# Kernel optimization log

Measured on AMD Instinct MI355X. Metric: run time of the kernel, lower is better.

Reference implementation:

```python
import jax, jax.numpy as jnp
import numpy as np

H = 2048          # hidden size
N_HEADS = 16
HEAD_DIM = H // N_HEADS   # 128
ATTN_SCALE = 8.0          # attention_scale > 1.0 -> custom max-subtract path
B, S = 2, 2048


def setup_inputs() -> dict:
    key = jax.random.key(0)
    k1, k2, k3, k4, k5 = jax.random.split(key, 5)
    hidden_states = jax.random.normal(k1, (B, S, H), dtype=jnp.float32)
    # causal left-to-right multiplicative mask, broadcast over batch and heads
    ltor_mask = jnp.tril(jnp.ones((S, S), dtype=jnp.float32))[None, None]
    std = 0.02
    W_qkv = jax.random.normal(k2, (H, 3 * H), dtype=jnp.float32) * std
    b_qkv = jnp.zeros((3 * H,), dtype=jnp.float32)
    W_out = jax.random.normal(k3, (H, H), dtype=jnp.float32) * std
    b_out = jnp.zeros((H,), dtype=jnp.float32)
    return {"hidden_states": hidden_states, "ltor_mask": ltor_mask,
            "W_qkv": W_qkv, "b_qkv": b_qkv, "W_out": W_out, "b_out": b_out}


def reference(hidden_states, ltor_mask, W_qkv, b_qkv, W_out, b_out):
    b, s, h = hidden_states.shape
    # fused QKV projection: [b, s, 3h]
    qkv = jnp.einsum('bsh,hk->bsk', hidden_states, W_qkv) + b_qkv
    q, k, v = jnp.split(qkv, 3, axis=-1)
    # [b, s, h] -> [b, n, s, hn]
    def to_heads(t):
        return t.reshape(b, s, N_HEADS, HEAD_DIM).transpose(0, 2, 1, 3)
    q, k, v = to_heads(q), to_heads(k), to_heads(v)
    # custom scale: q / sqrt(scale), k / sqrt(hn * scale)
    inv = 1.0 / (ATTN_SCALE * np.sqrt(np.float32(HEAD_DIM)))
    scores = jnp.einsum('bnqd,bnkd->bnqk', q, k) * jnp.float32(inv)
    # multiplicative mask BEFORE max-subtract (zeroes masked positions)
    scores = scores * ltor_mask
    # attention_scale > 1.0 path: subtract row max, re-multiply by scale
    scores = (scores - jnp.max(scores, axis=-1, keepdims=True)) * jnp.float32(ATTN_SCALE)
    # additive large-negative fill on masked entries
    scores = scores + jnp.float32(-65504.0) * (1.0 - ltor_mask)
    probs = jax.nn.softmax(scores, axis=-1)
    ctx = jnp.einsum('bnqk,bnkd->bnqd', probs, v)
    ctx = ctx.transpose(0, 2, 1, 3).reshape(b, s, h)
    out = jnp.einsum('bsh,hk->bsk', ctx, W_out) + b_out
    return out
```

## Files before the change

kernel.cpp:

```cpp
#include <hip/hip_runtime.h>

#define S_LEN 2048
#define HDIM  2048
#define NHEADS 16
#define DHEAD 128
#define BATCH 2
#define MROWS (BATCH * S_LEN)
#define QKVN  (3 * HDIM)

typedef _Float16 f16;
typedef _Float16 f16x8 __attribute__((ext_vector_type(8)));
typedef _Float16 f16x4 __attribute__((ext_vector_type(4)));
typedef float    f32x4 __attribute__((ext_vector_type(4)));
typedef float    f32x16 __attribute__((ext_vector_type(16)));

typedef const __attribute__((address_space(1))) void* gas_ptr;
typedef __attribute__((address_space(3))) void*       las_ptr;

#define MFMA16(a, b, c)  __builtin_amdgcn_mfma_f32_16x16x32_f16(a, b, c, 0, 0, 0)
#define MFMA32(a, b, c)  __builtin_amdgcn_mfma_f32_32x32x16_f16(a, b, c, 0, 0, 0)

__device__ __forceinline__ void gl_lds16(const f16* g, f16* lds_wave_base) {
#if defined(__has_builtin) && __has_builtin(__builtin_amdgcn_global_load_lds)
  __builtin_amdgcn_global_load_lds((gas_ptr)g, (las_ptr)lds_wave_base, 16, 0, 0);
#else
  int lane = threadIdx.x & 63;
  ((f16x8*)lds_wave_base)[lane] = *(const f16x8*)g;
#endif
}


__device__ __forceinline__ void transpose_tile(const float* __restrict__ W,
                                               f16* __restrict__ Wb,
                                               int K, int N, int k0, int n0,
                                               float* tile ) {
  int tr = threadIdx.x >> 4;
  int tc = (threadIdx.x & 15) * 4;
  int KT = K >> 5;
#pragma unroll
  for (int rr = 0; rr < 4; ++rr) {
    int r = rr * 16 + tr;
    float4 v = *(const float4*)(W + (size_t)(k0 + r) * N + n0 + tc);
    tile[r * 65 + tc + 0] = v.x; tile[r * 65 + tc + 1] = v.y;
    tile[r * 65 + tc + 2] = v.z; tile[r * 65 + tc + 3] = v.w;
  }
  __syncthreads();
#pragma unroll
  for (int rr = 0; rr < 4; ++rr) {
    int r = rr * 16 + tr;
    int n = n0 + r;
    int kBase = k0 + tc;
    f16x4 o;
#pragma unroll
    for (int c = 0; c < 4; ++c) o[c] = (f16)tile[(tc + c) * 65 + r];
    int nt = n >> 7, nn = n & 127;
    int kt = kBase >> 5, kc = (kBase >> 3) & 3, j = kBase & 7;
    *(f16x4*)(Wb + ((size_t)nt * KT + kt) * 4096 + (kc * 128 + nn) * 8 + j) = o;
  }
}

__global__ __launch_bounds__(256) void prep_kernel(const float* __restrict__ X,
                                                   f16* __restrict__ Xb,
                                                   const float* __restrict__ Wqkv,
                                                   f16* __restrict__ Wqkvb,
                                                   const float* __restrict__ Wout,
                                                   f16* __restrict__ Woutb) {
  __shared__ float tile[64 * 65];
  int bz = blockIdx.x;
  if (bz < 2048) {
    int kt = bz & 63, rt = bz >> 6;
    int t = threadIdx.x;
    int m = t >> 1, half = t & 1;
    const float* src = X + (size_t)(rt * 128 + m) * HDIM + kt * 32 + half * 16;
    float4 v0 = ((const float4*)src)[0];
    float4 v1 = ((const float4*)src)[1];
    float4 v2 = ((const float4*)src)[2];
    float4 v3 = ((const float4*)src)[3];
    f16x8 a = {(f16)v0.x, (f16)v0.y, (f16)v0.z, (f16)v0.w,
               (f16)v1.x, (f16)v1.y, (f16)v1.z, (f16)v1.w};
    f16x8 b = {(f16)v2.x, (f16)v2.y, (f16)v2.z, (f16)v2.w,
               (f16)v3.x, (f16)v3.y, (f16)v3.z, (f16)v3.w};
    f16* dst = Xb + ((size_t)rt * 64 + kt) * 4096 + ((half * 2) * 128 + m) * 8;
    *(f16x8*)dst = a;
    *(f16x8*)(dst + 1024) = b;
  } else if (bz < 5120) {
    int u = bz - 2048;
    int nx = u % 96, ky = u / 96;
    transpose_tile(Wqkv, Wqkvb, HDIM, QKVN, ky * 64, nx * 64, tile);
  } else {
    int u = bz - 5120;
    int nx = u & 31, ky = u >> 5;
    transpose_tile(Wout, Woutb, HDIM, HDIM, ky * 64, nx * 64, tile);
  }
}

template <int MODE>
__global__ __launch_bounds__(256) void gemm_kernel(const f16* __restrict__ Ablk,
                                                   const f16* __restrict__ Bblk,
                                                   const float* __restrict__ bias,
                                                   f16* __restrict__ Cpart,
                                                   f16* __restrict__ Qr,
                                                   f16* __restrict__ KB,
                                                   f16* __restrict__ VB,
                                                   int moff, int M, int N, int K) {
  __shared__ f16 As[4 * 128 * 8];
  __shared__ f16 Bs[4 * 128 * 8];
  int tid = threadIdx.x;
  int lane = tid & 63, w = tid >> 6;
  int lhi = lane >> 4, llo = lane & 15;
  int by = moff + blockIdx.y;
  int m0 = by * 128, n0 = blockIdx.x * 128;
  int wm = (w & 1) * 64, wn = (w >> 1) * 64;
  int KT = K >> 5;
  const f16* Ab = Ablk + (size_t)by * KT * 4096;
  const f16* Bb = Bblk + (size_t)blockIdx.x * KT * 4096;

  int ktBeg = 0, ktEnd = KT;
  if (MODE == 2) { int half = KT >> 1; ktBeg = blockIdx.z * half; ktEnd = ktBeg + half; }

  f32x4 acc[4][4];
#pragma unroll
  for (int i = 0; i < 4; ++i)
#pragma unroll
    for (int j = 0; j < 4; ++j) acc[i][j] = (f32x4){0.f, 0.f, 0.f, 0.f};

  for (int kt = ktBeg; kt < ktEnd; ++kt) {
    __syncthreads();
#pragma unroll
    for (int i2 = 0; i2 < 2; ++i2) {
      int Lw = i2 * 256 + w * 64;
      gl_lds16(Ab + (size_t)kt * 4096 + Lw * 8 + (lane * 8), As + Lw * 8);
      gl_lds16(Bb + (size_t)kt * 4096 + Lw * 8 + (lane * 8), Bs + Lw * 8);
    }
    __syncthreads();

    f16x8 af[4], bf[4];
#pragma unroll
    for (int i = 0; i < 4; ++i)
      af[i] = *(const f16x8*)(As + (lhi * 128 + wm + i * 16 + llo) * 8);
#pragma unroll
    for (int j = 0; j < 4; ++j)
      bf[j] = *(const f16x8*)(Bs + (lhi * 128 + wn + j * 16 + llo) * 8);
#pragma unroll
    for (int i = 0; i < 4; ++i)
#pragma unroll
      for (int j = 0; j < 4; ++j) acc[i][j] = MFMA16(af[i], bf[j], acc[i][j]);
  }

#pragma unroll
  for (int j = 0; j < 4; ++j) {
    int col = n0 + wn + j * 16 + llo;
    float bv = (MODE == 1) ? bias[col] : 0.f;
#pragma unroll
    for (int i = 0; i < 4; ++i) {
      int rowb = m0 + wm + i * 16 + lhi * 4;
      if (MODE == 2) {
        size_t zoff = (size_t)blockIdx.z * M * N;
#pragma unroll
        for (int r = 0; r < 4; ++r)
          Cpart[zoff + (size_t)(rowb + r) * N + col] = (f16)acc[i][j][r];
      } else {
        int region = n0 >> 11;
        if (region == 0) {
#pragma unroll
          for (int r = 0; r < 4; ++r)
            Qr[(size_t)(rowb + r) * HDIM + col] = (f16)(acc[i][j][r] + bv);
        } else if (region == 1) {
          int cK = col - HDIM;
          int hd = cK >> 7, d = cK & 127, g = d >> 3, dj = d & 7;
#pragma unroll
          for (int r = 0; r < 4; ++r) {
            int row = rowb + r;
            int b = row >> 11, s = row & 2047;
            int kt2 = s >> 6, key = s & 63;
            size_t addr = ((((size_t)(b * 16 + hd) * 32 + kt2) * 16 + g) * 64 + key) * 8 + dj;
            KB[addr] = (f16)(acc[i][j][r] + bv);
          }
        } else {
          int cV = col - 2 * HDIM;
          int hd = cV >> 7, d = cV & 127;
          int row = rowb;
          int b = row >> 11, s = row & 2047;
          int kt2 = s >> 6, key = s & 63;
          int kg = key >> 3, kj = key & 7;
          f16x4 pv = {(f16)(acc[i][j][0] + bv), (f16)(acc[i][j][1] + bv),
                      (f16)(acc[i][j][2] + bv), (f16)(acc[i][j][3] + bv)};
          size_t addr = ((((size_t)(b * 16 + hd) * 32 + kt2) * 8 + kg) * 128 + d) * 8 + kj;
          *(f16x4*)(VB + addr) = pv;
        }
      }
    }
  }
}

__global__ __launch_bounds__(256) void merge_out_kernel(const f16* __restrict__ Cpart,
                                                        const float* __restrict__ bias,
                                                        float* __restrict__ out) {
  int t = blockIdx.x * 256 + threadIdx.x;
  int col8 = (t & 255) * 8;
  int row = t >> 8;
  size_t base = (size_t)row * HDIM + col8;
  const size_t MN = (size_t)MROWS * HDIM;
  f16x8 a = *(const f16x8*)(Cpart + base);
  f16x8 b = *(const f16x8*)(Cpart + MN + base);
  float4 b0 = *(const float4*)(bias + col8);
  float4 b1 = *(const float4*)(bias + col8 + 4);
  float4 o0 = {(float)a[0] + (float)b[0] + b0.x, (float)a[1] + (float)b[1] + b0.y,
               (float)a[2] + (float)b[2] + b0.z, (float)a[3] + (float)b[3] + b0.w};
  float4 o1 = {(float)a[4] + (float)b[4] + b1.x, (float)a[5] + (float)b[5] + b1.y,
               (float)a[6] + (float)b[6] + b1.z, (float)a[7] + (float)b[7] + b1.w};
  *(float4*)(out + base) = o0;
  *(float4*)(out + base + 4) = o1;
}

__global__ __launch_bounds__(256, 3) void attn_kernel(const f16* __restrict__ Qr,
                                                      const f16* __restrict__ KB,
                                                      const f16* __restrict__ VB,
                                                      f16* __restrict__ Opart,
                                                      float* __restrict__ Lpart) {
  __shared__ f16 Ks[1024 * 8];
  __shared__ f16 Vs[1024 * 8];
  __shared__ f16 Ps[4][32 * 72];

  int tid = threadIdx.x, lane = tid & 63, w = tid >> 6;
  int l5 = lane & 31, hl = lane >> 5;
  int bh = blockIdx.y, b = bh >> 4, hd = bh & 15;
  int gx = blockIdx.x;
  int qt, kt0, kt1, slot;
  if (gx < 8) { qt = gx; slot = 0; kt0 = 0; kt1 = 2 * qt + 2; }
  else {
    qt = 8 + ((gx - 8) >> 1); slot = (gx - 8) & 1;
    kt0 = slot ? (qt + 1) : 0;
    kt1 = slot ? (2 * qt + 2) : (qt + 1);
  }

  int qbase = qt * 128 + w * 32;
  int qrow = qbase + l5;

  const f16* qp = Qr + (size_t)(b * S_LEN + qrow) * HDIM + hd * DHEAD + hl * 8;
  f16x8 qf[8];
#pragma unroll
  for (int s8 = 0; s8 < 8; ++s8) qf[s8] = *(const f16x8*)(qp + s8 * 16);

  f32x16 oac[4];
#pragma unroll
  for (int mt = 0; mt < 4; ++mt)
#pragma unroll
    for (int r = 0; r < 16; ++r) oac[mt][r] = 0.f;
  float rs = 0.f;

  const float C1 = 0.12752747419986393f;
  const float C2 = 11.541560327111708f;

  const f16* KBb = KB + (size_t)bh * 32 * 8192;
  const f16* VBb = VB + (size_t)bh * 32 * 8192;

  for (int kt = kt0; kt < kt1; ++kt) {
    __syncthreads();
    {
      const f16* Kt = KBb + (size_t)kt * 8192;
      const f16* Vt = VBb + (size_t)kt * 8192;
#pragma unroll
      for (int c = 0; c < 4; ++c) {
        int u0 = w * 256 + c * 64;
        gl_lds16(Kt + (size_t)(u0 + lane) * 8, Ks + u0 * 8);
        gl_lds16(Vt + (size_t)(u0 + lane) * 8, Vs + u0 * 8);
      }
    }
    __syncthreads();

    if (kt * 64 <= qbase + 31) {
      f32x16 sac[2];
#pragma unroll
      for (int mt = 0; mt < 2; ++mt)
#pragma unroll
        for (int r = 0; r < 16; ++r) sac[mt][r] = 0.f;
#pragma unroll
      for (int s8 = 0; s8 < 8; ++s8) {
#pragma unroll
        for (int mt = 0; mt < 2; ++mt) {
          f16x8 kf = *(const f16x8*)(Ks + ((s8 * 2 + hl) * 64 + mt * 32 + l5) * 8);
          sac[mt] = MFMA32(kf, qf[s8], sac[mt]);
        }
      }

      bool diag = (kt * 64 + 63 > qbase);
#pragma unroll
      for (int mt = 0; mt < 2; ++mt) {
#pragma unroll
        for (int g4 = 0; g4 < 4; ++g4) {
          f16x4 pk;
#pragma unroll
          for (int r = 0; r < 4; ++r) {
            int keyl = mt * 32 + g4 * 8 + hl * 4 + r;
            float p = __builtin_amdgcn_exp2f(fmaf(sac[mt][g4 * 4 + r], C1, -C2));
            if (diag && (kt * 64 + keyl > qrow)) p = 0.f;
            rs += p;
            pk[r] = (f16)p;
          }
          *(f16x4*)(&Ps[w][l5 * 72 + mt * 32 + g4 * 8 + hl * 4]) = pk;
        }
      }
      asm volatile("s_waitcnt lgkmcnt(0)" ::: "memory");

#pragma unroll
      for (int ks = 0; ks < 4; ++ks) {
        f16x8 pf = *(const f16x8*)(&Ps[w][l5 * 72 + ks * 16 + hl * 8]);
#pragma unroll
        for (int mt = 0; mt < 4; ++mt) {
          f16x8 vf = *(const f16x8*)(Vs + ((ks * 2 + hl) * 128 + mt * 32 + l5) * 8);
          oac[mt] = MFMA32(vf, pf, oac[mt]);
        }
      }
    }
  }

  float lsum = rs + __shfl_xor(rs, 32, 64);
  size_t ob = ((size_t)slot * 32 + bh) * S_LEN * DHEAD + (size_t)qrow * DHEAD;
#pragma unroll
  for (int mt = 0; mt < 4; ++mt) {
#pragma unroll
    for (int g4 = 0; g4 < 4; ++g4) {
      int d = mt * 32 + g4 * 8 + hl * 4;
      f16x4 ov = {(f16)oac[mt][g4 * 4 + 0], (f16)oac[mt][g4 * 4 + 1],
                  (f16)oac[mt][g4 * 4 + 2], (f16)oac[mt][g4 * 4 + 3]};
      *(f16x4*)(Opart + ob + d) = ov;
    }
  }
  if (hl == 0) Lpart[((size_t)slot * 32 + bh) * S_LEN + qrow] = lsum;
}

__global__ __launch_bounds__(256) void merge_kernel(const f16* __restrict__ Opart,
                                                    const float* __restrict__ Lpart,
                                                    f16* __restrict__ CTXb) {
  int t = blockIdx.x * 256 + threadIdx.x;
  int d8 = (t & 15) * 8;
  int q = (t >> 4) & 2047;
  int bh = t >> 15;
  int b = bh >> 4, hd = bh & 15;
  int ns = ((q >> 7) >= 8) ? 2 : 1;
  size_t o0 = ((size_t)bh * S_LEN + q) * DHEAD + d8;
  const size_t OSLOT = (size_t)32 * S_LEN * DHEAD;
  float l = Lpart[(size_t)bh * S_LEN + q];
  f16x8 a = *(const f16x8*)(Opart + o0);
  float acc[8];
#pragma unroll
  for (int j = 0; j < 8; ++j) acc[j] = (float)a[j];
  if (ns == 2) {
    l += Lpart[OSLOT / DHEAD + (size_t)bh * S_LEN + q];
    f16x8 a2 = *(const f16x8*)(Opart + OSLOT + o0);
#pragma unroll
    for (int j = 0; j < 8; ++j) acc[j] += (float)a2[j];
  }
  float inv = 1.0f / l;
  f16x8 o;
#pragma unroll
  for (int j = 0; j < 8; ++j) o[j] = (f16)(acc[j] * inv);
  int row = b * S_LEN + q;
  int col = hd * DHEAD + d8;
  int rt = row >> 7, rr = row & 127;
  int kt = col >> 5, kc = (col >> 3) & 3;
  *(f16x8*)(CTXb + ((size_t)rt * 64 + kt) * 4096 + (kc * 128 + rr) * 8) = o;
}

extern "C" void kernel_launch(void* const* d_in, const int* in_sizes, int n_in,
                              void* d_out, int out_size, void* d_ws, size_t ws_size,
                              hipStream_t stream) {
  const float* X    = (const float*)d_in[0];
  const float* Wqkv = (const float*)d_in[2];
  const float* bqkv = (const float*)d_in[3];
  const float* Wout = (const float*)d_in[4];
  const float* bout = (const float*)d_in[5];
  float* out = (float*)d_out;

  char* ws = (char*)d_ws;
  f16* Xb    = (f16*)ws;  ws += (size_t)MROWS * HDIM * sizeof(f16);
  f16* Wqkvb = (f16*)ws;  ws += (size_t)QKVN * HDIM * sizeof(f16);
  f16* Woutb = (f16*)ws;  ws += (size_t)HDIM * HDIM * sizeof(f16);
  f16* Qr    = (f16*)ws;  ws += (size_t)MROWS * HDIM * sizeof(f16);
  f16* KB    = (f16*)ws;  ws += (size_t)32 * 32 * 8192 * sizeof(f16);
  f16* VB    = (f16*)ws;  ws += (size_t)32 * 32 * 8192 * sizeof(f16);
  f16* Opart = (f16*)ws;  ws += (size_t)2 * 32 * S_LEN * DHEAD * sizeof(f16);
  float* Lpart = (float*)ws;  ws += (size_t)2 * 32 * S_LEN * sizeof(float);
  f16* CTXb  = Xb;
  f16* Cpart = Opart;

  prep_kernel<<<6144, 256, 0, stream>>>(X, Xb, Wqkv, Wqkvb, Wout, Woutb);

  gemm_kernel<1><<<dim3(QKVN / 128, 16), 256, 0, stream>>>(
      Xb, Wqkvb, bqkv, nullptr, Qr, KB, VB, 0, MROWS, QKVN, HDIM);
  gemm_kernel<1><<<dim3(QKVN / 128, 16), 256, 0, stream>>>(
      Xb, Wqkvb, bqkv, nullptr, Qr, KB, VB, 16, MROWS, QKVN, HDIM);

  attn_kernel<<<dim3(24, 32), 256, 0, stream>>>(Qr, KB, VB, Opart, Lpart);

  merge_kernel<<<(32 * S_LEN * 16) / 256, 256, 0, stream>>>(Opart, Lpart, CTXb);

  gemm_kernel<2><<<dim3(HDIM / 128, 32, 2), 256, 0, stream>>>(
      CTXb, Woutb, nullptr, Cpart, nullptr, nullptr, nullptr, 0, MROWS, HDIM, HDIM);

  merge_out_kernel<<<(MROWS * HDIM / 8) / 256, 256, 0, stream>>>(Cpart, bout, out);
}
```

Baseline: 425.4 us.

## Replace 128x128 GEMM with 256x256 tile, 4-stage async LDS pipeline

Swaps the GEMM kernel for a 512-thread, 256x256 output tile version. Global-to-LDS loads go through a 4-deep ring buffer with explicit vmcnt waits, interleaved barriers and raised wave priority around the MFMA sections. The QKV projection becomes a single launch instead of two half launches. This aims to cut global traffic per FLOP and hide load latency behind MFMA. The cost is much more LDS and more registers per block, which lowers occupancy, and fewer blocks for the output GEMM (256 blocks).

```diff
diff --git a/kernel.cpp b/kernel.cpp
--- a/kernel.cpp
+++ b/kernel.cpp
@@ -21,12 +21,7 @@
 #define MFMA32(a, b, c)  __builtin_amdgcn_mfma_f32_32x32x16_f16(a, b, c, 0, 0, 0)
 
 __device__ __forceinline__ void gl_lds16(const f16* g, f16* lds_wave_base) {
-#if defined(__has_builtin) && __has_builtin(__builtin_amdgcn_global_load_lds)
   __builtin_amdgcn_global_load_lds((gas_ptr)g, (las_ptr)lds_wave_base, 16, 0, 0);
-#else
-  int lane = threadIdx.x & 63;
-  ((f16x8*)lds_wave_base)[lane] = *(const f16x8*)g;
-#endif
 }
 
 
@@ -95,72 +90,107 @@
 }
 
 template <int MODE>
-__global__ __launch_bounds__(256) void gemm_kernel(const f16* __restrict__ Ablk,
-                                                   const f16* __restrict__ Bblk,
-                                                   const float* __restrict__ bias,
-                                                   f16* __restrict__ Cpart,
-                                                   f16* __restrict__ Qr,
-                                                   f16* __restrict__ KB,
-                                                   f16* __restrict__ VB,
-                                                   int moff, int M, int N, int K) {
-  __shared__ f16 As[4 * 128 * 8];
-  __shared__ f16 Bs[4 * 128 * 8];
-  int tid = threadIdx.x;
-  int lane = tid & 63, w = tid >> 6;
-  int lhi = lane >> 4, llo = lane & 15;
-  int by = moff + blockIdx.y;
-  int m0 = by * 128, n0 = blockIdx.x * 128;
-  int wm = (w & 1) * 64, wn = (w >> 1) * 64;
-  int KT = K >> 5;
-  const f16* Ab = Ablk + (size_t)by * KT * 4096;
-  const f16* Bb = Bblk + (size_t)blockIdx.x * KT * 4096;
-
-  int ktBeg = 0, ktEnd = KT;
-  if (MODE == 2) { int half = KT >> 1; ktBeg = blockIdx.z * half; ktEnd = ktBeg + half; }
-
-  f32x4 acc[4][4];
-#pragma unroll
-  for (int i = 0; i < 4; ++i)
+__global__ __launch_bounds__(512, 2) void gemm256_kernel(const f16* __restrict__ Ablk,
+                                                         const f16* __restrict__ Bblk,
+                                                         const float* __restrict__ bias,
+                                                         f16* __restrict__ Cpart,
+                                                         f16* __restrict__ Qr,
+                                                         f16* __restrict__ KB,
+                                                         f16* __restrict__ VB,
+                                                         int M, int N, int K) {
+  __shared__ f16 As[4][2][4096];
+  __shared__ f16 Bs[4][2][4096];
+  const int tid = threadIdx.x;
+  const int lane = tid & 63, wv = tid >> 6;
+  const int lhi = lane >> 4, llo = lane & 15;
+  const int wr = wv >> 2, wc = wv & 3;
+  const int bx = blockIdx.x, by = blockIdx.y;
+  const int KT = K >> 5;
+  int t0 = 0, ntiles = KT;
+  if (MODE == 2) { ntiles = KT >> 1; t0 = blockIdx.z * ntiles; }
+
+  const f16* Ab0 = Ablk + ((size_t)(2 * by)     * KT + t0) * 4096;
+  const f16* Ab1 = Ablk + ((size_t)(2 * by + 1) * KT + t0) * 4096;
+  const f16* Bb0 = Bblk + ((size_t)(2 * bx)     * KT + t0) * 4096;
+  const f16* Bb1 = Bblk + ((size_t)(2 * bx + 1) * KT + t0) * 4096;
+
+  f32x4 acc[8][4];
+#pragma unroll
+  for (int i = 0; i < 8; ++i)
 #pragma unroll
     for (int j = 0; j < 4; ++j) acc[i][j] = (f32x4){0.f, 0.f, 0.f, 0.f};
 
-  for (int kt = ktBeg; kt < ktEnd; ++kt) {
-    __syncthreads();
-#pragma unroll
-    for (int i2 = 0; i2 < 2; ++i2) {
-      int Lw = i2 * 256 + w * 64;
-      gl_lds16(Ab + (size_t)kt * 4096 + Lw * 8 + (lane * 8), As + Lw * 8);
-      gl_lds16(Bb + (size_t)kt * 4096 + Lw * 8 + (lane * 8), Bs + Lw * 8);
-    }
-    __syncthreads();
-
-    f16x8 af[4], bf[4];
+  auto stA = [&](int bufi, int kt) {
+    gl_lds16(Ab0 + (size_t)kt * 4096 + tid * 8, &As[bufi][0][0] + wv * 512);
+    gl_lds16(Ab1 + (size_t)kt * 4096 + tid * 8, &As[bufi][1][0] + wv * 512);
+  };
+  auto stB = [&](int bufi, int kt) {
+    gl_lds16(Bb0 + (size_t)kt * 4096 + tid * 8, &Bs[bufi][0][0] + wv * 512);
+    gl_lds16(Bb1 + (size_t)kt * 4096 + tid * 8, &Bs[bufi][1][0] + wv * 512);
+  };
+
+#pragma unroll
+  for (int u = 0; u < 3; ++u) { stA(u, u); stB(u, u); }
+
+  for (int t = 0; t < ntiles; ++t) {
+    const int buf = t & 3;
+    const bool st = (t + 3 < ntiles);
+    const int nb = (t + 3) & 3, ntile = t + 3;
+
+    if (t + 2 < ntiles)      asm volatile("s_waitcnt vmcnt(8)" ::: "memory");
+    else if (t + 1 < ntiles) asm volatile("s_waitcnt vmcnt(4)" ::: "memory");
+    else                     asm volatile("s_waitcnt vmcnt(0)" ::: "memory");
+    __builtin_amdgcn_s_barrier();
+
+    const f16* Ah = &As[buf][wr][0];
+    const f16* Bh = &Bs[buf][wc >> 1][0];
+    f16x8 bfr[4], afr[4];
+
+#pragma unroll
+    for (int j = 0; j < 4; ++j)
+      bfr[j] = *(const f16x8*)(Bh + (lhi * 128 + (wc & 1) * 64 + j * 16 + llo) * 8);
 #pragma unroll
     for (int i = 0; i < 4; ++i)
-      af[i] = *(const f16x8*)(As + (lhi * 128 + wm + i * 16 + llo) * 8);
-#pragma unroll
-    for (int j = 0; j < 4; ++j)
-      bf[j] = *(const f16x8*)(Bs + (lhi * 128 + wn + j * 16 + llo) * 8);
+      afr[i] = *(const f16x8*)(Ah + (lhi * 128 + i * 16 + llo) * 8);
+    if (st) stA(nb, ntile);
+    __builtin_amdgcn_s_barrier();
+    asm volatile("s_waitcnt lgkmcnt(0)" ::: "memory");
+    __builtin_amdgcn_s_setprio(1);
 #pragma unroll
     for (int i = 0; i < 4; ++i)
 #pragma unroll
-      for (int j = 0; j < 4; ++j) acc[i][j] = MFMA16(af[i], bf[j], acc[i][j]);
+      for (int j = 0; j < 4; ++j) acc[i][j] = MFMA16(afr[i], bfr[j], acc[i][j]);
+    __builtin_amdgcn_s_setprio(0);
+    __builtin_amdgcn_s_barrier();
+
+#pragma unroll
+    for (int i = 0; i < 4; ++i)
+      afr[i] = *(const f16x8*)(Ah + (lhi * 128 + (i + 4) * 16 + llo) * 8);
+    if (st) stB(nb, ntile);
+    __builtin_amdgcn_s_barrier();
+    asm volatile("s_waitcnt lgkmcnt(0)" ::: "memory");
+    __builtin_amdgcn_s_setprio(1);
+#pragma unroll
+    for (int i = 0; i < 4; ++i)
+#pragma unroll
+      for (int j = 0; j < 4; ++j) acc[i + 4][j] = MFMA16(afr[i], bfr[j], acc[i + 4][j]);
+    __builtin_amdgcn_s_setprio(0);
   }
 
 #pragma unroll
   for (int j = 0; j < 4; ++j) {
-    int col = n0 + wn + j * 16 + llo;
+    int col = bx * 256 + wc * 64 + j * 16 + llo;
     float bv = (MODE == 1) ? bias[col] : 0.f;
 #pragma unroll
-    for (int i = 0; i < 4; ++i) {
-      int rowb = m0 + wm + i * 16 + lhi * 4;
+    for (int i = 0; i < 8; ++i) {
+      int rowb = by * 256 + wr * 128 + i * 16 + lhi * 4;
       if (MODE == 2) {
         size_t zoff = (size_t)blockIdx.z * M * N;
 #pragma unroll
         for (int r = 0; r < 4; ++r)
           Cpart[zoff + (size_t)(rowb + r) * N + col] = (f16)acc[i][j][r];
       } else {
-        int region = n0 >> 11;
+        int region = col >> 11;
         if (region == 0) {
 #pragma unroll
           for (int r = 0; r < 4; ++r)
@@ -387,17 +417,15 @@
 
   prep_kernel<<<6144, 256, 0, stream>>>(X, Xb, Wqkv, Wqkvb, Wout, Woutb);
 
-  gemm_kernel<1><<<dim3(QKVN / 128, 16), 256, 0, stream>>>(
-      Xb, Wqkvb, bqkv, nullptr, Qr, KB, VB, 0, MROWS, QKVN, HDIM);
-  gemm_kernel<1><<<dim3(QKVN / 128, 16), 256, 0, stream>>>(
-      Xb, Wqkvb, bqkv, nullptr, Qr, KB, VB, 16, MROWS, QKVN, HDIM);
+  gemm256_kernel<1><<<dim3(QKVN / 256, MROWS / 256), 512, 0, stream>>>(
+      Xb, Wqkvb, bqkv, nullptr, Qr, KB, VB, MROWS, QKVN, HDIM);
 
   attn_kernel<<<dim3(24, 32), 256, 0, stream>>>(Qr, KB, VB, Opart, Lpart);
 
   merge_kernel<<<(32 * S_LEN * 16) / 256, 256, 0, stream>>>(Opart, Lpart, CTXb);
 
-  gemm_kernel<2><<<dim3(HDIM / 128, 32, 2), 256, 0, stream>>>(
-      CTXb, Woutb, nullptr, Cpart, nullptr, nullptr, nullptr, 0, MROWS, HDIM, HDIM);
+  gemm256_kernel<2><<<dim3(HDIM / 256, MROWS / 256, 2), 512, 0, stream>>>(
+      CTXb, Woutb, nullptr, Cpart, nullptr, nullptr, nullptr, MROWS, HDIM, HDIM);
 
   merge_out_kernel<<<(MROWS * HDIM / 8) / 256, 256, 0, stream>>>(Cpart, bout, out);
 }
```

Measured after the change: 406.8 us. -4.4%, faster.
